# Optimization experiments

Measured on AMD Instinct MI355X. Metric: run time of the kernel, lower is better.

## Reference

```python
import jax, jax.numpy as jnp
import numpy as np

B, S, D, H = 4, 2048, 1024, 16
DK = D // H

def setup_inputs() -> dict:
    key = jax.random.key(0)
    ks = jax.random.split(key, 8)
    scale = 1.0 / np.sqrt(D)
    return {
        "q": jax.random.normal(ks[0], (B, S, D), jnp.float32),
        "k": jax.random.normal(ks[1], (B, S, D), jnp.float32),
        "v": jax.random.normal(ks[2], (B, S, D), jnp.float32),
        "wq": jax.random.normal(ks[3], (D, D), jnp.float32) * scale,
        "bq": jnp.zeros((D,), jnp.float32),
        "wk": jax.random.normal(ks[4], (D, D), jnp.float32) * scale,
        "bk": jnp.zeros((D,), jnp.float32),
        "wv": jax.random.normal(ks[5], (D, D), jnp.float32) * scale,
        "bv": jnp.zeros((D,), jnp.float32),
        "wo": jax.random.normal(ks[6], (D, D), jnp.float32) * scale,
        "bo": jnp.zeros((D,), jnp.float32),
    }

def reference(q, k, v, wq, bq, wk, bk, wv, bv, wo, bo):
    b, s, _ = q.shape
    # projections; split heads -> [b, h, s, d_k]
    def proj(x, w, bias):
        y = x @ w + bias
        return y.reshape(b, -1, H, DK).transpose(0, 2, 1, 3)
    qh, kh, vh = proj(q, wq, bq), proj(k, wk, bk), proj(v, wv, bv)
    scores = jnp.einsum("bhqd,bhkd->bhqk", qh, kh) / np.sqrt(DK).astype(jnp.float32)
    attn = jax.nn.softmax(scores, axis=-1)  # dropout = identity (eval mode)
    out = jnp.einsum("bhqk,bhkd->bhqd", attn, vh)
    out = out.transpose(0, 2, 1, 3).reshape(b, s, D)
    return out @ wo + bo
```

## Files before the change

kernel.cpp:

```cpp
#include <hip/hip_runtime.h>
#include <hip/hip_bf16.h>

#define B_   4
#define S_   2048
#define D_   1024
#define H_   16
#define DK_  64
#define NTOK 8192

typedef __bf16 bf16_t;
typedef __bf16 bf16x8 __attribute__((ext_vector_type(8)));
typedef __bf16 bf16x4 __attribute__((ext_vector_type(4)));
typedef __bf16 bf16x2 __attribute__((ext_vector_type(2)));
typedef float  f32x4  __attribute__((ext_vector_type(4)));
typedef float  f32x16 __attribute__((ext_vector_type(16)));
typedef unsigned u32x4 __attribute__((ext_vector_type(4)));
typedef int    i32x2  __attribute__((ext_vector_type(2)));

__device__ __forceinline__ void gll16(const void* g, void* l) {
  __builtin_amdgcn_global_load_lds(
      (const __attribute__((address_space(1))) void*)g,
      (__attribute__((address_space(3))) void*)l,
      16, 0, 0);
}

__device__ __forceinline__ f32x4 mfma32(bf16x8 a, bf16x8 b, f32x4 c) {
  return __builtin_amdgcn_mfma_f32_16x16x32_bf16(a, b, c, 0, 0, 0);
}

__device__ __forceinline__ f32x16 mfma32x32(bf16x8 a, bf16x8 b, f32x16 c) {
#if defined(__HIP_DEVICE_COMPILE__)
  return __builtin_amdgcn_mfma_f32_32x32x16_bf16(a, b, c, 0, 0, 0);
#else
  (void)a; (void)b;
  return c;
#endif
}

__device__ __forceinline__ float fast_exp2(float x) {
#if defined(__HIP_DEVICE_COMPILE__) && __has_builtin(__builtin_amdgcn_exp2f)
  return __builtin_amdgcn_exp2f(x);
#else
  return exp2f(x);
#endif
}

__device__ __forceinline__ f32x16 zero16() {
  f32x16 z;
#pragma unroll
  for (int i = 0; i < 16; ++i) z[i] = 0.f;
  return z;
}

__device__ __forceinline__ unsigned pkbf(float lo, float hi) {
  bf16x2 t;
  t[0] = (bf16_t)lo;
  t[1] = (bf16_t)hi;
  return __builtin_bit_cast(unsigned, t);
}

__device__ __forceinline__ void plswap(unsigned &x, unsigned &y) {
#if defined(__HIP_DEVICE_COMPILE__)
  i32x2 r = __builtin_amdgcn_permlane32_swap((int)x, (int)y, false, false);
  x = (unsigned)r[0];
  y = (unsigned)r[1];
#endif
}

__device__ __forceinline__ void build_pa(const f32x16 s, bf16x8 &p0, bf16x8 &p1) {
  unsigned A0 = pkbf(fast_exp2(s[0]),  fast_exp2(s[1]));
  unsigned A1 = pkbf(fast_exp2(s[2]),  fast_exp2(s[3]));
  unsigned B0 = pkbf(fast_exp2(s[4]),  fast_exp2(s[5]));
  unsigned B1 = pkbf(fast_exp2(s[6]),  fast_exp2(s[7]));
  unsigned C0 = pkbf(fast_exp2(s[8]),  fast_exp2(s[9]));
  unsigned C1 = pkbf(fast_exp2(s[10]), fast_exp2(s[11]));
  unsigned D0 = pkbf(fast_exp2(s[12]), fast_exp2(s[13]));
  unsigned D1 = pkbf(fast_exp2(s[14]), fast_exp2(s[15]));
  plswap(A0, B0);
  plswap(A1, B1);
  plswap(C0, D0);
  plswap(C1, D1);
  u32x4 lo = {A0, A1, B0, B1};
  u32x4 hi = {C0, C1, D0, D1};
  p0 = __builtin_bit_cast(bf16x8, lo);
  p1 = __builtin_bit_cast(bf16x8, hi);
}

__global__ __launch_bounds__(256) void prep_weights(
    const float* __restrict__ wq, const float* __restrict__ wk,
    const float* __restrict__ wv, const float* __restrict__ wo,
    bf16_t* __restrict__ wtHi) {
  const int z = blockIdx.z;
  const float* W = (z == 0) ? wq : (z == 1) ? wk : (z == 2) ? wv : wo;
  const int k0 = blockIdx.x * 64;
  const int n0 = blockIdx.y * 64;
  const int t = threadIdx.x;
  __shared__ float T[64][65];
#pragma unroll
  for (int rr = 0; rr < 4; ++rr) {
    int row = rr * 16 + (t >> 4);
    int cc = (t & 15) * 4;
    const float4 v = *(const float4*)&W[(size_t)(k0 + row) * D_ + n0 + cc];
    T[row][cc + 0] = v.x; T[row][cc + 1] = v.y;
    T[row][cc + 2] = v.z; T[row][cc + 3] = v.w;
  }
  __syncthreads();
  const int n = t >> 2;
  const int kc = (t & 3) * 16;
  bf16x8 h0, h1;
#pragma unroll
  for (int j = 0; j < 16; ++j) {
    float vv = T[kc + j][n];
    if (j < 8) h0[j] = (bf16_t)vv;
    else       h1[j - 8] = (bf16_t)vv;
  }
  size_t ofs = (size_t)z * 1048576 + (size_t)(n0 + n) * D_ + k0 + kc;
  *(bf16x8*)&wtHi[ofs] = h0; *(bf16x8*)&wtHi[ofs + 8] = h1;
}

__global__ __launch_bounds__(256) void gemm_qkv_fused(
    const float* __restrict__ Aq, const float* __restrict__ Ak,
    const float* __restrict__ Av,
    const float* __restrict__ bq, const float* __restrict__ bk,
    const float* __restrict__ bv,
    const bf16_t* __restrict__ wtHi, bf16_t* __restrict__ outQKV) {
  const int z = blockIdx.z;
  const float* A    = (z == 0) ? Aq : (z == 1) ? Ak : Av;
  const float* bias = (z == 0) ? bq : (z == 1) ? bk : bv;
  const bf16_t* WHi = wtHi + (size_t)z * 1048576;
  bf16_t* Out = outQKV + (size_t)z * 8388608;

  const int row0 = blockIdx.x * 128;
  const int col0 = blockIdx.y * 128;
  const int t = threadIdx.x;
  const int w = t >> 6, L = t & 63;
  const int m = L & 15, g = L >> 4;

  __shared__ __align__(16) bf16_t As2[128 * 64];
  __shared__ __align__(16) bf16_t Whi_s[128 * 64];

  f32x4 acc[4][4];
#pragma unroll
  for (int i = 0; i < 4; ++i)
#pragma unroll
    for (int j = 0; j < 4; ++j) acc[i][j] = (f32x4){0.f, 0.f, 0.f, 0.f};

  const int aw0 = (w & 1) * 64;
  const int bw0 = (w >> 1) * 64;

  int srow[4], scol[4];
#pragma unroll
  for (int i = 0; i < 4; ++i) {
    int slot = i * 256 + t;
    srow[i] = slot >> 3;
    scol[i] = (slot & 7) ^ (srow[i] & 7);
  }

  for (int kt = 0; kt < 16; ++kt) {
    const int k0 = kt * 64;
#pragma unroll
    for (int i = 0; i < 4; ++i) {
      const float* src = &A[(size_t)(row0 + srow[i]) * D_ + k0 + scol[i] * 8];
      f32x4 x0 = *(const f32x4*)src;
      f32x4 x1 = *(const f32x4*)(src + 4);
      u32x4 pk = {pkbf(x0[0], x0[1]), pkbf(x0[2], x0[3]),
                  pkbf(x1[0], x1[1]), pkbf(x1[2], x1[3])};
      *(u32x4*)&As2[(i * 256 + t) * 8] = pk;
    }
#pragma unroll
    for (int i = 0; i < 4; ++i) {
      gll16(&WHi[(size_t)(col0 + srow[i]) * D_ + k0 + scol[i] * 8],
            &Whi_s[i * 2048 + w * 512]);
    }
    __syncthreads();

#pragma unroll
    for (int kh = 0; kh < 2; ++kh) {
      bf16x8 af[4], wh[4];
#pragma unroll
      for (int it = 0; it < 4; ++it) {
        int row = aw0 + it * 16 + m;
        int sl = ((kh * 4 + g) ^ (m & 7)) * 8;
        af[it] = *(const bf16x8*)&As2[row * 64 + sl];
      }
#pragma unroll
      for (int jt = 0; jt < 4; ++jt) {
        int n = bw0 + jt * 16 + m;
        int sl = ((kh * 4 + g) ^ (m & 7)) * 8;
        wh[jt] = *(const bf16x8*)&Whi_s[n * 64 + sl];
      }
#pragma unroll
      for (int it = 0; it < 4; ++it)
#pragma unroll
        for (int jt = 0; jt < 4; ++jt)
          acc[it][jt] = mfma32(af[it], wh[jt], acc[it][jt]);
    }
    __syncthreads();
  }
#pragma unroll
  for (int jt = 0; jt < 4; ++jt) {
    int col = col0 + bw0 + jt * 16 + m;
    float bcol = bias[col];
    int h = col >> 6, d = col & 63;
#pragma unroll
    for (int it = 0; it < 4; ++it) {
      if (z != 2) {
#pragma unroll
        for (int r = 0; r < 4; ++r) {
          int row = row0 + aw0 + it * 16 + g * 4 + r;
          int b = row >> 11, s = row & 2047;
          Out[((size_t)((b * H_ + h) * S_ + s)) * DK_ + d] =
              (bf16_t)(acc[it][jt][r] + bcol);
        }
      } else {
        int row = row0 + aw0 + it * 16 + g * 4;
        int b = row >> 11, s = row & 2047;
        bf16x4 p4;
#pragma unroll
        for (int r = 0; r < 4; ++r) p4[r] = (bf16_t)(acc[it][jt][r] + bcol);
        *(bf16x4*)&Out[((size_t)((b * H_ + h) * DK_ + d)) * S_ + s] = p4;
      }
    }
  }
}

__global__ __launch_bounds__(256, 2) void attn(
    const bf16_t* __restrict__ Qh, const bf16_t* __restrict__ Kh,
    const bf16_t* __restrict__ VhT, bf16_t* __restrict__ Ohi) {
  const int bh = blockIdx.y;
  const int q0 = blockIdx.x * 128;
  const int t = threadIdx.x, w = t >> 6;
  const int lane = t & 63;
  const int lo5 = lane & 31, hi = lane >> 5;

  __shared__ __align__(16) bf16_t Ks[64 * 64];
  __shared__ __align__(16) bf16_t Vt[64 * 64];

  const size_t qbase = (size_t)bh * S_ * DK_;
  const size_t vbase = (size_t)bh * DK_ * S_;

  const int qrow = q0 + w * 32 + lo5;
  bf16x8 qf[4];
#pragma unroll
  for (int ks = 0; ks < 4; ++ks) {
    bf16x8 v = *(const bf16x8*)&Qh[qbase + (size_t)qrow * DK_ + ks * 16 + hi * 8];
#pragma unroll
    for (int j = 0; j < 8; ++j) v[j] = (bf16_t)(0.18033688f * (float)v[j]);
    qf[ks] = v;
  }

  bf16x8 ones;
#pragma unroll
  for (int j = 0; j < 8; ++j) ones[j] = (bf16_t)1.f;

  int offs[4];
#pragma unroll
  for (int ks = 0; ks < 4; ++ks)
    offs[ks] = lo5 * 64 + (((ks * 2 + hi) ^ (lo5 & 7)) * 8);

  f32x16 oacc0 = zero16(), oacc1 = zero16(), lacc = zero16();

  for (int kv0 = 0; kv0 < S_; kv0 += 64) {
#pragma unroll
    for (int rr = 0; rr < 2; ++rr) {
      int lin16 = rr * 256 + t;
      int rrow = lin16 >> 3;
      int c = (lin16 & 7) ^ (rrow & 7);
      gll16(&Kh[qbase + (size_t)(kv0 + rrow) * DK_ + c * 8], &Ks[rr * 2048 + w * 512]);
      gll16(&VhT[vbase + (size_t)rrow * S_ + kv0 + c * 8], &Vt[rr * 2048 + w * 512]);
    }
    __syncthreads();

    f32x16 sc0 = zero16(), sc1 = zero16();
#pragma unroll
    for (int ks = 0; ks < 4; ++ks) {
      bf16x8 k0 = *(const bf16x8*)&Ks[offs[ks]];
      bf16x8 k1 = *(const bf16x8*)&Ks[offs[ks] + 2048];
      sc0 = mfma32x32(k0, qf[ks], sc0);
      sc1 = mfma32x32(k1, qf[ks], sc1);
    }

    bf16x8 pa0, pa1, pa2, pa3;
    build_pa(sc0, pa0, pa1);
    build_pa(sc1, pa2, pa3);

#pragma unroll
    for (int ks = 0; ks < 4; ++ks) {
      bf16x8 pb = (ks == 0) ? pa0 : (ks == 1) ? pa1 : (ks == 2) ? pa2 : pa3;
      lacc = mfma32x32(ones, pb, lacc);
      bf16x8 v0 = *(const bf16x8*)&Vt[offs[ks]];
      bf16x8 v1 = *(const bf16x8*)&Vt[offs[ks] + 2048];
      oacc0 = mfma32x32(v0, pb, oacc0);
      oacc1 = mfma32x32(v1, pb, oacc1);
    }
    __syncthreads();
  }

  const int b = bh >> 4, h = bh & 15;
  const float inv = 1.f / lacc[0];
  const size_t rowofs = ((size_t)(b * S_ + qrow)) * D_ + h * DK_;
#pragma unroll
  for (int rg = 0; rg < 4; ++rg) {
    bf16x4 o0, o1;
#pragma unroll
    for (int j = 0; j < 4; ++j) {
      o0[j] = (bf16_t)(oacc0[rg * 4 + j] * inv);
      o1[j] = (bf16_t)(oacc1[rg * 4 + j] * inv);
    }
    *(bf16x4*)&Ohi[rowofs + rg * 8 + hi * 4] = o0;
    *(bf16x4*)&Ohi[rowofs + 32 + rg * 8 + hi * 4] = o1;
  }
}

__global__ __launch_bounds__(256) void gemm_out(
    const bf16_t* __restrict__ Ahi, const bf16_t* __restrict__ wtHi,
    const float* __restrict__ bias, float* __restrict__ Out) {
  const bf16_t* WHi = wtHi + (size_t)3 * 1048576;
  const int row0 = blockIdx.x * 128;
  const int col0 = blockIdx.y * 128;
  const int t = threadIdx.x;
  const int w = t >> 6, L = t & 63;
  const int m = L & 15, g = L >> 4;

  __shared__ __align__(16) bf16_t Ahi_s[128 * 64];
  __shared__ __align__(16) bf16_t Whi_s[128 * 64];

  f32x4 acc[4][4];
#pragma unroll
  for (int i = 0; i < 4; ++i)
#pragma unroll
    for (int j = 0; j < 4; ++j) acc[i][j] = (f32x4){0.f, 0.f, 0.f, 0.f};

  const int aw0 = (w & 1) * 64;
  const int bw0 = (w >> 1) * 64;

  int srow[4], scol[4];
#pragma unroll
  for (int i = 0; i < 4; ++i) {
    int slot = i * 256 + t;
    srow[i] = slot >> 3;
    scol[i] = (slot & 7) ^ (srow[i] & 7);
  }

  for (int kt = 0; kt < 16; ++kt) {
    const int k0 = kt * 64;
#pragma unroll
    for (int i = 0; i < 4; ++i) {
      gll16(&Ahi[(size_t)(row0 + srow[i]) * D_ + k0 + scol[i] * 8],
            &Ahi_s[i * 2048 + w * 512]);
      gll16(&WHi[(size_t)(col0 + srow[i]) * D_ + k0 + scol[i] * 8],
            &Whi_s[i * 2048 + w * 512]);
    }
    __syncthreads();

#pragma unroll
    for (int kh = 0; kh < 2; ++kh) {
      bf16x8 ah[4], wh[4];
#pragma unroll
      for (int it = 0; it < 4; ++it) {
        int row = aw0 + it * 16 + m;
        int sl = ((kh * 4 + g) ^ (m & 7)) * 8;
        ah[it] = *(const bf16x8*)&Ahi_s[row * 64 + sl];
      }
#pragma unroll
      for (int jt = 0; jt < 4; ++jt) {
        int n = bw0 + jt * 16 + m;
        int sl = ((kh * 4 + g) ^ (m & 7)) * 8;
        wh[jt] = *(const bf16x8*)&Whi_s[n * 64 + sl];
      }
#pragma unroll
      for (int it = 0; it < 4; ++it)
#pragma unroll
        for (int jt = 0; jt < 4; ++jt)
          acc[it][jt] = mfma32(ah[it], wh[jt], acc[it][jt]);
    }
    __syncthreads();
  }
#pragma unroll
  for (int jt = 0; jt < 4; ++jt) {
    int col = col0 + bw0 + jt * 16 + m;
    float bcol = bias[col];
#pragma unroll
    for (int it = 0; it < 4; ++it)
#pragma unroll
      for (int r = 0; r < 4; ++r) {
        int row = row0 + aw0 + it * 16 + g * 4 + r;
        Out[(size_t)row * D_ + col] = acc[it][jt][r] + bcol;
      }
  }
}

extern "C" void kernel_launch(void* const* d_in, const int* in_sizes, int n_in,
                              void* d_out, int out_size, void* d_ws, size_t ws_size,
                              hipStream_t stream) {
  const float* q  = (const float*)d_in[0];
  const float* k  = (const float*)d_in[1];
  const float* v  = (const float*)d_in[2];
  const float* wq = (const float*)d_in[3];
  const float* bq = (const float*)d_in[4];
  const float* wk = (const float*)d_in[5];
  const float* bk = (const float*)d_in[6];
  const float* wv = (const float*)d_in[7];
  const float* bv = (const float*)d_in[8];
  const float* wo = (const float*)d_in[9];
  const float* bo = (const float*)d_in[10];
  float* out = (float*)d_out;

  char* ws = (char*)d_ws;
  bf16_t* wtHi = (bf16_t*)(ws);
  bf16_t* QKVh = (bf16_t*)(ws + (8ull << 20));
  bf16_t* Ohi  = (bf16_t*)(ws + (56ull << 20));

  hipLaunchKernelGGL(prep_weights, dim3(16, 16, 4), dim3(256), 0, stream,
                     wq, wk, wv, wo, wtHi);
  hipLaunchKernelGGL(gemm_qkv_fused, dim3(64, 8, 3), dim3(256), 0, stream,
                     q, k, v, bq, bk, bv, wtHi, QKVh);
  hipLaunchKernelGGL(attn, dim3(16, 64), dim3(256), 0, stream,
                     QKVh, QKVh + 8388608, QKVh + 16777216, Ohi);
  hipLaunchKernelGGL(gemm_out, dim3(64, 8), dim3(256), 0, stream,
                     Ohi, wtHi, bo, out);
}
```

Measured before the change: 354.1 us.

## Double-buffer LDS tiles in fused QKV GEMM to overlap loads with MFMA

Adds ping-pong shared-memory buffers for the A and weight tiles in the fused QKV projection GEMM. The next k-tile's fp32 activations are prefetched into registers and the weights go by global_load_lds into the alternate buffer while MFMAs run on the current one, with bf16 conversion and the LDS store done after the compute. This removes one barrier per iteration and hides global load latency, at the cost of doubled LDS use (64KB) and extra registers, which may lower occupancy.

```diff
diff --git a/kernel.cpp b/kernel.cpp
--- a/kernel.cpp
+++ b/kernel.cpp
@@ -136,8 +136,8 @@
   const int w = t >> 6, L = t & 63;
   const int m = L & 15, g = L >> 4;
 
-  __shared__ __align__(16) bf16_t As2[128 * 64];
-  __shared__ __align__(16) bf16_t Whi_s[128 * 64];
+  __shared__ __align__(16) bf16_t As2[2][128 * 64];
+  __shared__ __align__(16) bf16_t Whi_s[2][128 * 64];
 
   f32x4 acc[4][4];
 #pragma unroll
@@ -156,24 +156,48 @@
     scol[i] = (slot & 7) ^ (srow[i] & 7);
   }
 
+  f32x4 rA[8];
+
+#pragma unroll
+  for (int i = 0; i < 4; ++i) {
+    const float* src = &A[(size_t)(row0 + srow[i]) * D_ + scol[i] * 8];
+    rA[2 * i]     = *(const f32x4*)src;
+    rA[2 * i + 1] = *(const f32x4*)(src + 4);
+  }
+#pragma unroll
+  for (int i = 0; i < 4; ++i) {
+    u32x4 pk = {pkbf(rA[2 * i][0], rA[2 * i][1]),
+                pkbf(rA[2 * i][2], rA[2 * i][3]),
+                pkbf(rA[2 * i + 1][0], rA[2 * i + 1][1]),
+                pkbf(rA[2 * i + 1][2], rA[2 * i + 1][3])};
+    *(u32x4*)&As2[0][(i * 256 + t) * 8] = pk;
+  }
+#pragma unroll
+  for (int i = 0; i < 4; ++i)
+    gll16(&WHi[(size_t)(col0 + srow[i]) * D_ + scol[i] * 8],
+          &Whi_s[0][i * 2048 + w * 512]);
+  __syncthreads();
+
   for (int kt = 0; kt < 16; ++kt) {
-    const int k0 = kt * 64;
-#pragma unroll
-    for (int i = 0; i < 4; ++i) {
-      const float* src = &A[(size_t)(row0 + srow[i]) * D_ + k0 + scol[i] * 8];
-      f32x4 x0 = *(const f32x4*)src;
-      f32x4 x1 = *(const f32x4*)(src + 4);
-      u32x4 pk = {pkbf(x0[0], x0[1]), pkbf(x0[2], x0[3]),
-                  pkbf(x1[0], x1[1]), pkbf(x1[2], x1[3])};
-      *(u32x4*)&As2[(i * 256 + t) * 8] = pk;
-    }
-#pragma unroll
-    for (int i = 0; i < 4; ++i) {
-      gll16(&WHi[(size_t)(col0 + srow[i]) * D_ + k0 + scol[i] * 8],
-            &Whi_s[i * 2048 + w * 512]);
-    }
-    __syncthreads();
-
+    const int c = kt & 1;
+    const bool more = (kt < 15);
+    const int k1 = (kt + 1) * 64;
+
+    if (more) {
+#pragma unroll
+      for (int i = 0; i < 4; ++i) {
+        const float* src = &A[(size_t)(row0 + srow[i]) * D_ + k1 + scol[i] * 8];
+        rA[2 * i]     = *(const f32x4*)src;
+        rA[2 * i + 1] = *(const f32x4*)(src + 4);
+      }
+#pragma unroll
+      for (int i = 0; i < 4; ++i)
+        gll16(&WHi[(size_t)(col0 + srow[i]) * D_ + k1 + scol[i] * 8],
+              &Whi_s[c ^ 1][i * 2048 + w * 512]);
+    }
+
+    const bf16_t* as_b = &As2[c][0];
+    const bf16_t* ws_b = &Whi_s[c][0];
 #pragma unroll
     for (int kh = 0; kh < 2; ++kh) {
       bf16x8 af[4], wh[4];
@@ -181,13 +205,13 @@
       for (int it = 0; it < 4; ++it) {
         int row = aw0 + it * 16 + m;
         int sl = ((kh * 4 + g) ^ (m & 7)) * 8;
-        af[it] = *(const bf16x8*)&As2[row * 64 + sl];
+        af[it] = *(const bf16x8*)&as_b[row * 64 + sl];
       }
 #pragma unroll
       for (int jt = 0; jt < 4; ++jt) {
         int n = bw0 + jt * 16 + m;
         int sl = ((kh * 4 + g) ^ (m & 7)) * 8;
-        wh[jt] = *(const bf16x8*)&Whi_s[n * 64 + sl];
+        wh[jt] = *(const bf16x8*)&ws_b[n * 64 + sl];
       }
 #pragma unroll
       for (int it = 0; it < 4; ++it)
@@ -195,8 +219,20 @@
         for (int jt = 0; jt < 4; ++jt)
           acc[it][jt] = mfma32(af[it], wh[jt], acc[it][jt]);
     }
+
+    if (more) {
+#pragma unroll
+      for (int i = 0; i < 4; ++i) {
+        u32x4 pk = {pkbf(rA[2 * i][0], rA[2 * i][1]),
+                    pkbf(rA[2 * i][2], rA[2 * i][3]),
+                    pkbf(rA[2 * i + 1][0], rA[2 * i + 1][1]),
+                    pkbf(rA[2 * i + 1][2], rA[2 * i + 1][3])};
+        *(u32x4*)&As2[c ^ 1][(i * 256 + t) * 8] = pk;
+      }
+    }
     __syncthreads();
   }
+
 #pragma unroll
   for (int jt = 0; jt < 4; ++jt) {
     int col = col0 + bw0 + jt * 16 + m;
```

Result: slower. 373.8 us (+5.6%).
